# Kernel optimization log

Measured on AMD Instinct MI355X. Metric: run time of the kernel, lower is better.

Reference implementation:

```python
import jax, jax.numpy as jnp
import numpy as np

D_MODEL = 1024
NHEAD = 16
HEAD_DIM = D_MODEL // NHEAD
ROPE_BASE = 10000.0


def rotate_half(x):
    h = x.shape[-1] // 2
    return jnp.concatenate((-x[..., h:], x[..., :h]), axis=-1)


def rope_cos_sin(seq_len, dim, dtype):
    inv_freq = 1.0 / (ROPE_BASE ** (jnp.arange(0, dim, 2, dtype=jnp.float32) / dim))
    t = jnp.arange(seq_len, dtype=jnp.float32)
    freqs = jnp.einsum('i,j->ij', t, inv_freq)  # [S, dim/2]
    emb = jnp.concatenate((freqs, freqs), axis=-1)  # [S, dim]
    return jnp.cos(emb).astype(dtype), jnp.sin(emb).astype(dtype)


def setup_inputs() -> dict:
    key = jax.random.key(0)
    ks = jax.random.split(key, 9)
    b, s = 2, 2048
    lim = 1.0 / np.sqrt(D_MODEL)
    def lin(kw, kb):
        W = jax.random.uniform(kw, (D_MODEL, D_MODEL), jnp.float32, -lim, lim)
        bia = jax.random.uniform(kb, (D_MODEL,), jnp.float32, -lim, lim)
        return W, bia
    Wq, bq = lin(ks[0], ks[1])
    Wk, bk = lin(ks[2], ks[3])
    Wv, bv = lin(ks[4], ks[5])
    Wo, bo = lin(ks[6], ks[7])
    x = jax.random.normal(ks[8], (b, s, D_MODEL), jnp.float32)
    return {"x": x, "Wq": Wq, "bq": bq, "Wk": Wk, "bk": bk,
            "Wv": Wv, "bv": bv, "Wo": Wo, "bo": bo}


def reference(x, Wq, bq, Wk, bk, Wv, bv, Wo, bo):
    b, s, _ = x.shape
    scale = jnp.sqrt(jnp.asarray(HEAD_DIM, x.dtype))
    # projections (torch Linear: y = x @ W.T + b)
    q = x @ Wq.T + bq
    k = x @ Wk.T + bk
    v = x @ Wv.T + bv
    # [b, h, s, d]
    def split_heads(t):
        return t.reshape(b, s, NHEAD, HEAD_DIM).transpose(0, 2, 1, 3)
    q, k, v = split_heads(q), split_heads(k), split_heads(v)
    cos, sin = rope_cos_sin(s, HEAD_DIM, x.dtype)  # [s, d]
    q = q * cos + rotate_half(q) * sin
    k = k * cos + rotate_half(k) * sin
    scores = jnp.einsum('bhqd,bhkd->bhqk', q, k) / scale
    probs = jax.nn.softmax(scores, axis=-1)
    out = jnp.einsum('bhqk,bhkd->bhqd', probs, v)
    out = out.transpose(0, 2, 1, 3).reshape(b, s, D_MODEL)
    return out @ Wo.T + bo
```

## Files before the change

kernel.cpp:

```cpp
#include <hip/hip_runtime.h>
#include <hip/hip_bf16.h>
#include <stdint.h>


typedef __attribute__((ext_vector_type(8))) short bf16x8;
typedef __attribute__((ext_vector_type(4))) float f32x4;
typedef __attribute__((ext_vector_type(16))) float f32x16;
typedef __attribute__((ext_vector_type(4))) short short4v;
typedef __attribute__((ext_vector_type(4))) float float4v;
typedef __attribute__((ext_vector_type(4))) unsigned uint32x4;

#define DEV __device__ __forceinline__

DEV short f2bf(float f) {
  union { float f; uint32_t u; } v; v.f = f;
  uint32_t r = (v.u + 0x7fffu + ((v.u >> 16) & 1u)) >> 16;
  return (short)(uint16_t)r;
}
DEV float bf2f(short b) {
  union { uint32_t u; float f; } v; v.u = ((uint32_t)(uint16_t)b) << 16;
  return v.f;
}
DEV unsigned cvtpk(float a, float b) {
  unsigned d;
  asm("v_cvt_pk_bf16_f32 %0, %1, %2" : "=v"(d) : "v"(a), "v"(b));
  return d;
}
DEV void gload16(const void* g, const void* l) {
  __builtin_amdgcn_global_load_lds((const __attribute__((address_space(1))) void*)g,
                                   (__attribute__((address_space(3))) void*)l, 16, 0, 0);
}

__global__ void convert_kernel(const float* __restrict__ x,
                               const float* __restrict__ wq, const float* __restrict__ wk,
                               const float* __restrict__ wv, const float* __restrict__ wo,
                               short* __restrict__ xb, short* __restrict__ wqb,
                               short* __restrict__ wkb, short* __restrict__ wvb,
                               short* __restrict__ wob) {
  const int idx = blockIdx.x * blockDim.x + threadIdx.x;
  const float* src; short* dst; int off;
  if (idx < 1048576)      { src = x;  dst = xb;  off = idx; }
  else if (idx < 1310720) { src = wq; dst = wqb; off = idx - 1048576; }
  else if (idx < 1572864) { src = wk; dst = wkb; off = idx - 1310720; }
  else if (idx < 1835008) { src = wv; dst = wvb; off = idx - 1572864; }
  else                    { src = wo; dst = wob; off = idx - 1835008; }
  float4v v = *(const float4v*)(src + (size_t)off * 4);
  short4v o;
  o[0] = f2bf(v[0]); o[1] = f2bf(v[1]); o[2] = f2bf(v[2]); o[3] = f2bf(v[3]);
  *(short4v*)(dst + (size_t)off * 4) = o;
}

__global__ void rope_table_kernel(float* __restrict__ ct, float* __restrict__ st) {
  const int idx = blockIdx.x * blockDim.x + threadIdx.x;
  const int t = idx >> 5, j = idx & 31;
  const float f = (float)t * exp2f(-(float)j * (13.287712379549449f / 32.f));
  ct[idx] = cosf(f);
  st[idx] = sinf(f);
}

template<bool FINAL>
__global__ __launch_bounds__(256, 2) void gemm_bt(
    const short* __restrict__ A,
    const short* __restrict__ W0, const short* __restrict__ W1, const short* __restrict__ W2,
    const float* __restrict__ b0, const float* __restrict__ b1, const float* __restrict__ b2,
    short* __restrict__ o0, short* __restrict__ o1, short* __restrict__ o2,
    float* __restrict__ of,
    const float* __restrict__ ct, const float* __restrict__ st) {
  constexpr int K = 1024;
  __shared__ short lds[2 * 128 * 64];
  short* As = lds;
  short* Ws = lds + 128 * 64;

  const int tid = threadIdx.x;
  const int lane = tid & 63;
  const int w = tid >> 6;
  const int wr = w >> 1, wc = w & 1;
  const int bn = blockIdx.x, bm = blockIdx.y, z = blockIdx.z;

  const short* Wt = (z == 0) ? W0 : (z == 1 ? W1 : W2);
  const float* bias = (z == 0) ? b0 : (z == 1 ? b1 : b2);
  short* ob = (z == 0) ? o0 : (z == 1 ? o1 : o2);

  const int lrow = lane >> 3;
  const int clog = 16 * ((lane & 7) ^ lrow);

  f32x4 acc[4][4] = {};
  const size_t arowbase = (size_t)(bm * 128) * K;
  const size_t wrowbase = (size_t)(bn * 128) * K;

  for (int kt = 0; kt < K / 64; ++kt) {
    __syncthreads();
#pragma unroll
    for (int i = 0; i < 4; ++i) {
      const int c = i * 4 + w;
      const int row = c * 8 + lrow;
      gload16(A + arowbase + (size_t)row * K + kt * 64 + (clog >> 1),
              (const char*)As + c * 1024);
      gload16(Wt + wrowbase + (size_t)row * K + kt * 64 + (clog >> 1),
              (const char*)Ws + c * 1024);
    }
    __syncthreads();
#pragma unroll
    for (int kk = 0; kk < 2; ++kk) {
      bf16x8 af[4], bf[4];
      const int kb = (kk * 32 + (lane >> 4) * 8) * 2;
#pragma unroll
      for (int mi = 0; mi < 4; ++mi) {
        const int row = wr * 64 + mi * 16 + (lane & 15);
        af[mi] = *(const bf16x8*)((const char*)As + row * 128 + (kb ^ ((row & 7) << 4)));
      }
#pragma unroll
      for (int ni = 0; ni < 4; ++ni) {
        const int row = wc * 64 + ni * 16 + (lane & 15);
        bf[ni] = *(const bf16x8*)((const char*)Ws + row * 128 + (kb ^ ((row & 7) << 4)));
      }
#pragma unroll
      for (int mi = 0; mi < 4; ++mi)
#pragma unroll
        for (int ni = 0; ni < 4; ++ni)
          acc[mi][ni] = __builtin_amdgcn_mfma_f32_16x16x32_bf16(af[mi], bf[ni], acc[mi][ni], 0, 0, 0);
    }
  }

  float bv[4];
#pragma unroll
  for (int ni = 0; ni < 4; ++ni)
    bv[ni] = bias[bn * 128 + wc * 64 + ni * 16 + (lane & 15)];

#pragma unroll
  for (int mi = 0; mi < 4; ++mi) {
#pragma unroll
    for (int r = 0; r < 4; ++r) {
      const int m = bm * 128 + wr * 64 + mi * 16 + (lane >> 4) * 4 + r;
      float v[4];
#pragma unroll
      for (int ni = 0; ni < 4; ++ni) v[ni] = acc[mi][ni][r] + bv[ni];
      if (!FINAL && z < 2) {
        const int s = m & 2047;
        const float sc = (z == 0) ? 0.18033688011f : 1.0f;
#pragma unroll
        for (int jj = 0; jj < 2; ++jj) {
          const int j = jj * 16 + (lane & 15);
          const float c = ct[s * 32 + j] * sc, sn = st[s * 32 + j] * sc;
          const float a = v[jj], bb = v[jj + 2];
          v[jj]     = a * c - bb * sn;
          v[jj + 2] = bb * c + a * sn;
        }
      }
#pragma unroll
      for (int ni = 0; ni < 4; ++ni) {
        const int n = bn * 128 + wc * 64 + ni * 16 + (lane & 15);
        if (FINAL) {
          of[(size_t)m * 1024 + n] = v[ni];
        } else {
          const int b = m >> 11, s = m & 2047, h = n >> 6, d = n & 63;
          ob[(((size_t)(b * 16 + h)) * 2048 + s) * 64 + d] = f2bf(v[ni]);
        }
      }
    }
  }
}

__global__ void vtrans_kernel(const short* __restrict__ v, short* __restrict__ vt) {
  __shared__ short t[64][72];
  const int bh = blockIdx.x, st0 = blockIdx.y * 64;
  const int tid = threadIdx.x;
#pragma unroll
  for (int i = 0; i < 2; ++i) {
    const int j = i * 256 + tid;
    const int row = j >> 3, c8 = (j & 7) * 8;
    *(bf16x8*)&t[row][c8] = *(const bf16x8*)(v + (((size_t)bh * 2048) + st0 + row) * 64 + c8);
  }
  __syncthreads();
#pragma unroll
  for (int i = 0; i < 2; ++i) {
    const int j = i * 256 + tid;
    const int dd = j >> 3, s8 = (j & 7) * 8;
    const int b16 = s8 & ~15;
    const int hi8 = (s8 >> 3) & 1;
    bf16x8 o;
#pragma unroll
    for (int e = 0; e < 8; ++e)
      o[e] = t[b16 + 4 * hi8 + (e & 3) + 8 * (e >> 2)][dd];
    *(bf16x8*)(vt + (((size_t)bh * 64) + dd) * 2048 + st0 + s8) = o;
  }
}

__global__ __launch_bounds__(512, 4) void attn_kernel(
    const short* __restrict__ q, const short* __restrict__ k,
    const short* __restrict__ vt, short* __restrict__ ao) {
  __shared__ char ldsb[65536];

  const int tid = threadIdx.x, lane = tid & 63, w = tid >> 6;
  const int wg = w & 3, g = w >> 2;
  const int hi = lane >> 5;
  const int bh = blockIdx.x, qt = blockIdx.y;
  const int lrow = lane >> 3;
  const int cshort = 8 * ((lane & 7) ^ lrow);

  const int qrow = qt * 128 + wg * 32 + (lane & 31);
  const short* qb = q + ((size_t)bh * 2048 + qrow) * 64 + hi * 8;
  bf16x8 qf[4];
#pragma unroll
  for (int m = 0; m < 4; ++m) qf[m] = *(const bf16x8*)(qb + 16 * m);

  bf16x8 ones;
#pragma unroll
  for (int j = 0; j < 8; ++j) ones[j] = (short)0x3F80;

  f32x16 acc[2] = {};
  f32x16 lacc = {};

  char* gbase = ldsb + g * 32768;
  const size_t kvoff = (size_t)g * 1024;

  const int c0 = wg, c1 = 4 + wg, c2 = 8 + wg, c3 = 12 + wg;
  const short* kp0 = k + ((size_t)bh * 2048 + kvoff + c0 * 8 + lrow) * 64 + cshort;
  const short* kp1 = k + ((size_t)bh * 2048 + kvoff + c1 * 8 + lrow) * 64 + cshort;
  const short* vp0 = vt + ((size_t)bh * 64 + (c2 - 8) * 8 + lrow) * 2048 + kvoff + cshort;
  const short* vp1 = vt + ((size_t)bh * 64 + (c3 - 8) * 8 + lrow) * 2048 + kvoff + cshort;

  gload16(kp0, gbase + c0 * 1024);
  gload16(kp1, gbase + c1 * 1024);
  gload16(vp0, gbase + c2 * 1024);
  gload16(vp1, gbase + c3 * 1024);
  kp0 += 4096; kp1 += 4096; vp0 += 64; vp1 += 64;
  __syncthreads();

  int cur = 0;
  for (int j = 0; j < 16; ++j) {
    if (j < 15) {
      char* nb = gbase + (cur ^ 1) * 16384;
      gload16(kp0, nb + c0 * 1024);
      gload16(kp1, nb + c1 * 1024);
      gload16(vp0, nb + c2 * 1024);
      gload16(vp1, nb + c3 * 1024);
      kp0 += 4096; kp1 += 4096; vp0 += 64; vp1 += 64;
    }

    const char* kb_ = gbase + cur * 16384;
    const char* vb_ = kb_ + 8192;

    f32x16 stv[2] = {};
#pragma unroll
    for (int m = 0; m < 4; ++m) {
      const int bc = 32 * m + 16 * hi;
#pragma unroll
      for (int t = 0; t < 2; ++t) {
        const int row = t * 32 + (lane & 31);
        bf16x8 kf = *(const bf16x8*)(kb_ + row * 128 + (bc ^ ((row & 7) << 4)));
        stv[t] = __builtin_amdgcn_mfma_f32_32x32x16_bf16(kf, qf[m], stv[t], 0, 0, 0);
      }
    }

#pragma unroll
    for (int t = 0; t < 2; ++t)
#pragma unroll
      for (int r = 0; r < 16; ++r)
        stv[t][r] = __builtin_amdgcn_exp2f(stv[t][r]);

#pragma unroll
    for (int sg = 0; sg < 4; ++sg) {
      const int t = sg >> 1, sl = sg & 1;
      uint32x4 pu;
#pragma unroll
      for (int jj = 0; jj < 4; ++jj)
        pu[jj] = cvtpk(stv[t][8 * sl + 2 * jj], stv[t][8 * sl + 2 * jj + 1]);
      bf16x8 pv8 = __builtin_bit_cast(bf16x8, pu);
      const int base = 64 * t + 32 * sl + 16 * hi;
#pragma unroll
      for (int db = 0; db < 2; ++db) {
        const int row = db * 32 + (lane & 31);
        const int sw = (row & 7) << 4;
        bf16x8 vv = *(const bf16x8*)(vb_ + row * 128 + (base ^ sw));
        acc[db] = __builtin_amdgcn_mfma_f32_32x32x16_bf16(vv, pv8, acc[db], 0, 0, 0);
      }
      lacc = __builtin_amdgcn_mfma_f32_32x32x16_bf16(ones, pv8, lacc, 0, 0, 0);
    }

    __syncthreads();
    cur ^= 1;
  }

  float* fm = (float*)(void*)ldsb + wg * 2112;
  if (g == 1) {
    fm[lane] = lacc[0];
#pragma unroll
    for (int db = 0; db < 2; ++db)
#pragma unroll
      for (int r = 0; r < 16; ++r)
        fm[64 + (db * 16 + r) * 64 + lane] = acc[db][r];
  }
  __syncthreads();

  if (g == 0) {
    const float rl = 1.0f / (lacc[0] + fm[lane]);
    const int b = bh >> 4, h = bh & 15;
    short* orow = ao + ((size_t)b * 2048 + qrow) * 1024 + h * 64;
#pragma unroll
    for (int db = 0; db < 2; ++db)
#pragma unroll
      for (int gq = 0; gq < 4; ++gq) {
        short4v o;
#pragma unroll
        for (int jj = 0; jj < 4; ++jj) {
          const int r = 4 * gq + jj;
          const float v1 = fm[64 + (db * 16 + r) * 64 + lane];
          o[jj] = f2bf((acc[db][r] + v1) * rl);
        }
        *(short4v*)(orow + db * 32 + 8 * gq + 4 * hi) = o;
      }
  }
}

extern "C" void kernel_launch(void* const* d_in, const int* in_sizes, int n_in,
                              void* d_out, int out_size, void* d_ws, size_t ws_size,
                              hipStream_t stream) {
  const float* x  = (const float*)d_in[0];
  const float* Wq = (const float*)d_in[1];
  const float* bq = (const float*)d_in[2];
  const float* Wk = (const float*)d_in[3];
  const float* bk = (const float*)d_in[4];
  const float* Wv = (const float*)d_in[5];
  const float* bv = (const float*)d_in[6];
  const float* Wo = (const float*)d_in[7];
  const float* bo = (const float*)d_in[8];
  float* out = (float*)d_out;

  char* ws = (char*)d_ws;
  short* xb  = (short*)(ws);
  short* wqb = (short*)(ws + 8388608);
  short* wkb = (short*)(ws + 10485760);
  short* wvb = (short*)(ws + 12582912);
  short* wob = (short*)(ws + 14680064);
  float* ct  = (float*)(ws + 16777216);
  float* st  = (float*)(ws + 17039360);
  short* qb  = (short*)(ws + 17301504);
  short* kb  = (short*)(ws + 25690112);
  short* vb  = (short*)(ws + 34078720);
  short* vtb = (short*)(ws + 42467328);
  short* ab  = (short*)(ws + 50855936);

  convert_kernel<<<dim3(8192), dim3(256), 0, stream>>>(x, Wq, Wk, Wv, Wo, xb, wqb, wkb, wvb, wob);
  rope_table_kernel<<<dim3(256), dim3(256), 0, stream>>>(ct, st);
  gemm_bt<false><<<dim3(8, 32, 3), dim3(256), 0, stream>>>(
      xb, wqb, wkb, wvb, bq, bk, bv, qb, kb, vb, (float*)nullptr, ct, st);
  vtrans_kernel<<<dim3(32, 32), dim3(256), 0, stream>>>(vb, vtb);
  attn_kernel<<<dim3(32, 16), dim3(512), 0, stream>>>(qb, kb, vtb, ab);
  gemm_bt<true><<<dim3(8, 32, 1), dim3(256), 0, stream>>>(
      ab, wob, (short*)nullptr, (short*)nullptr, bo, (float*)nullptr, (float*)nullptr,
      (short*)nullptr, (short*)nullptr, (short*)nullptr, out, ct, st);
}
```

Before: 114.5 us.

## Halve attention block to 64 query rows with 4 waves, doubling grid

Measured after the change: 115.0 us. No clear change (+0.4%).

```diff
diff --git a/kernel.cpp b/kernel.cpp
--- a/kernel.cpp
+++ b/kernel.cpp
@@ -186,19 +186,19 @@
   }
 }
 
-__global__ __launch_bounds__(512, 4) void attn_kernel(
+__global__ __launch_bounds__(256, 2) void attn_kernel(
     const short* __restrict__ q, const short* __restrict__ k,
     const short* __restrict__ vt, short* __restrict__ ao) {
   __shared__ char ldsb[65536];
 
   const int tid = threadIdx.x, lane = tid & 63, w = tid >> 6;
-  const int wg = w & 3, g = w >> 2;
+  const int wg = w & 1, g = w >> 1;
   const int hi = lane >> 5;
   const int bh = blockIdx.x, qt = blockIdx.y;
   const int lrow = lane >> 3;
   const int cshort = 8 * ((lane & 7) ^ lrow);
 
-  const int qrow = qt * 128 + wg * 32 + (lane & 31);
+  const int qrow = qt * 64 + wg * 32 + (lane & 31);
   const short* qb = q + ((size_t)bh * 2048 + qrow) * 64 + hi * 8;
   bf16x8 qf[4];
 #pragma unroll
@@ -214,28 +214,34 @@
   char* gbase = ldsb + g * 32768;
   const size_t kvoff = (size_t)g * 1024;
 
-  const int c0 = wg, c1 = 4 + wg, c2 = 8 + wg, c3 = 12 + wg;
-  const short* kp0 = k + ((size_t)bh * 2048 + kvoff + c0 * 8 + lrow) * 64 + cshort;
-  const short* kp1 = k + ((size_t)bh * 2048 + kvoff + c1 * 8 + lrow) * 64 + cshort;
-  const short* vp0 = vt + ((size_t)bh * 64 + (c2 - 8) * 8 + lrow) * 2048 + kvoff + cshort;
-  const short* vp1 = vt + ((size_t)bh * 64 + (c3 - 8) * 8 + lrow) * 2048 + kvoff + cshort;
-
-  gload16(kp0, gbase + c0 * 1024);
-  gload16(kp1, gbase + c1 * 1024);
-  gload16(vp0, gbase + c2 * 1024);
-  gload16(vp1, gbase + c3 * 1024);
-  kp0 += 4096; kp1 += 4096; vp0 += 64; vp1 += 64;
+  const short* kp = k + ((size_t)bh * 2048 + kvoff + (wg * 4) * 8 + lrow) * 64 + cshort;
+  const short* vp[4];
+#pragma unroll
+  for (int i = 0; i < 4; ++i)
+    vp[i] = vt + ((size_t)bh * 64 + (wg * 4 + i) * 8 + lrow) * 2048 + kvoff + cshort;
+
+#pragma unroll
+  for (int i = 0; i < 4; ++i) {
+    gload16(kp + i * 512, gbase + (wg * 4 + i) * 1024);
+    gload16(vp[i], gbase + 8192 + (wg * 4 + i) * 1024);
+  }
+  kp += 4096;
+#pragma unroll
+  for (int i = 0; i < 4; ++i) vp[i] += 64;
   __syncthreads();
 
   int cur = 0;
   for (int j = 0; j < 16; ++j) {
     if (j < 15) {
       char* nb = gbase + (cur ^ 1) * 16384;
-      gload16(kp0, nb + c0 * 1024);
-      gload16(kp1, nb + c1 * 1024);
-      gload16(vp0, nb + c2 * 1024);
-      gload16(vp1, nb + c3 * 1024);
-      kp0 += 4096; kp1 += 4096; vp0 += 64; vp1 += 64;
+#pragma unroll
+      for (int i = 0; i < 4; ++i) {
+        gload16(kp + i * 512, nb + (wg * 4 + i) * 1024);
+        gload16(vp[i], nb + 8192 + (wg * 4 + i) * 1024);
+      }
+      kp += 4096;
+#pragma unroll
+      for (int i = 0; i < 4; ++i) vp[i] += 64;
     }
 
     const char* kb_ = gbase + cur * 16384;
@@ -346,7 +352,7 @@
   gemm_bt<false><<<dim3(8, 32, 3), dim3(256), 0, stream>>>(
       xb, wqb, wkb, wvb, bq, bk, bv, qb, kb, vb, (float*)nullptr, ct, st);
   vtrans_kernel<<<dim3(32, 32), dim3(256), 0, stream>>>(vb, vtb);
-  attn_kernel<<<dim3(32, 16), dim3(512), 0, stream>>>(qb, kb, vtb, ab);
+  attn_kernel<<<dim3(32, 32), dim3(256), 0, stream>>>(qb, kb, vtb, ab);
   gemm_bt<true><<<dim3(8, 32, 1), dim3(256), 0, stream>>>(
       ab, wob, (short*)nullptr, (short*)nullptr, bo, (float*)nullptr, (float*)nullptr,
       (short*)nullptr, (short*)nullptr, (short*)nullptr, out, ct, st);
```
